# Performance work log

Hardware: AMD Instinct MI355X
Metric: run time of the kernel (lower is better)

Reference implementation:

```python
import jax, jax.numpy as jnp
import numpy as np

# Hard-coded constants from the original module
GAMMA = 0.1      # self.gamma default
N_STEPS = 10     # self.n_steps default
RHO = 0.9        # RMSProp decay
LR = 0.009       # RMSProp learning rate
MOM = 0.9        # momentum
EPS = 1e-8       # RMSProp epsilon
ABS_EPS = 1e-6   # diff_abs smoothing: diff_abs(x) = sqrt(x^2 + 1e-6)

B, IN_DIM, OUT_DIM = 4096, 2048, 4096


def setup_inputs() -> dict:
    key = jax.random.key(0)
    k1, k2 = jax.random.split(key)
    inputs = jax.random.normal(k1, (B, IN_DIM), dtype=jnp.float32)
    # keras 'uniform' init: U(-0.05, 0.05), shape (output_dim, input_dim)
    W = jax.random.uniform(k2, (OUT_DIM, IN_DIM), minval=-0.05, maxval=0.05, dtype=jnp.float32)
    return {"inputs": inputs, "W": W}


def reference(inputs, W):
    batch = inputs.shape[0]
    out_dim = W.shape[0]
    a = jnp.sqrt(inputs * inputs + ABS_EPS)          # diff_abs(inputs), [B, in_dim]
    act = lambda u: 0.5 * (1.0 + jnp.exp(-u))        # self.activation

    def cost(x):
        # l1_norm.sum() + l1_inov + own_norm  (prior = 0)
        l1 = (GAMMA * act(x @ W) * a).sum()
        l1_inov = (GAMMA / 10.0) * jnp.sum(x * x)
        own = GAMMA * jnp.sum(jnp.sqrt(x * x + ABS_EPS))
        return l1 + l1_inov + own

    grad_cost = jax.grad(cost)

    def step(carry, _):
        x, acc1, acc2 = carry
        g = grad_cost(x)                              # [B, out_dim]
        new_acc1 = RHO * acc1 + (1.0 - RHO) * g * g
        denom = jnp.sqrt(new_acc1 + EPS)
        new_acc2 = MOM * acc2 - LR * g / denom
        cand = x - LR * g / denom
        t = 0.1 * LR / denom                          # elementwise prox threshold
        new_x = jnp.maximum(cand - t, 0.0) + jnp.minimum(cand + t, 0.0) + MOM * new_acc2
        new_x = jax.lax.stop_gradient(new_x)          # theano disconnected_grad
        return (new_x, new_acc1, new_acc2), None

    z = jnp.zeros((batch, out_dim), dtype=inputs.dtype)
    # scan runs n_steps; last step's l1_norm uses the state after n_steps-1 updates,
    # so run n_steps-1 updates then compute the final l1_norm directly.
    (x, _, _), _ = jax.lax.scan(step, (z, z, z), None, length=N_STEPS - 1)
    return GAMMA * act(x @ W) * a                     # outputs[-1][-1]: last l1_norm, [B, in_dim]
```

## Files before the change

### kernel.cpp

```cpp
#include <hip/hip_runtime.h>
#include <cstdint>
#include <cstddef>

#define B_DIM   4096
#define IN_DIM  2048
#define OUT_DIM 4096

typedef __attribute__((ext_vector_type(8))) __bf16 bf16x8;
typedef __attribute__((ext_vector_type(4))) float  f32x4;
typedef unsigned short ushortT;

__device__ __forceinline__ ushortT f2bf(float f) {
    unsigned int u = __float_as_uint(f);
    u += 0x7FFFu + ((u >> 16) & 1u);
    return (ushortT)(u >> 16);
}
__device__ __forceinline__ float bf2f(ushortT b) {
    return __uint_as_float(((unsigned int)b) << 16);
}

__device__ __forceinline__ void gload16(const void* g, void* l) {
    __builtin_amdgcn_global_load_lds(
        (const __attribute__((address_space(1))) void*)g,
        (__attribute__((address_space(3))) void*)l, 16, 0, 0);
}

__global__ void prep_g0_kernel(const float* __restrict__ in, ushortT* __restrict__ Gb) {
    int i = blockIdx.x * 256 + threadIdx.x;
    float4 v = reinterpret_cast<const float4*>(in)[i];
    ushort4 g;
    g.x = f2bf(-0.05f * sqrtf(v.x * v.x + 1e-6f));
    g.y = f2bf(-0.05f * sqrtf(v.y * v.y + 1e-6f));
    g.z = f2bf(-0.05f * sqrtf(v.z * v.z + 1e-6f));
    g.w = f2bf(-0.05f * sqrtf(v.w * v.w + 1e-6f));
    reinterpret_cast<ushort4*>(Gb)[i] = g;
}

__global__ void conv_w_kernel(const float* __restrict__ W, ushortT* __restrict__ Wb,
                              ushortT* __restrict__ WTb) {
    __shared__ float tile[64][65];
    const int i0 = blockIdx.x * 64;
    const int j0 = blockIdx.y * 64;
    const int c  = threadIdx.x & 63;
    const int rq = threadIdx.x >> 6;
#pragma unroll
    for (int rp = 0; rp < 16; ++rp) {
        int row = rp * 4 + rq;
        float w = W[(size_t)(j0 + row) * IN_DIM + i0 + c];
        tile[row][c] = w;
        Wb[(size_t)(j0 + row) * IN_DIM + i0 + c] = f2bf(w);
    }
    __syncthreads();
#pragma unroll
    for (int rp = 0; rp < 16; ++rp) {
        int row = rp * 4 + rq;
        WTb[(size_t)(i0 + row) * OUT_DIM + j0 + c] = f2bf(tile[c][row]);
    }
}

template <int EPI, int BM>
__global__ __launch_bounds__(512, 2)
void gemm_ring(const ushortT* __restrict__ A, const ushortT* __restrict__ Bm,
               int N, int K,
               const float* __restrict__ inb, ushortT* __restrict__ Gb,
               float* __restrict__ out,
               float* __restrict__ x, ushortT* __restrict__ acc1,
               ushortT* __restrict__ acc2, ushortT* __restrict__ xb) {
    constexpr int BN   = 256;
    constexpr int ASZ  = BM * 64;
    constexpr int BSZ  = BN * 64;
    constexpr int SLOT = ASZ + BSZ;
    constexpr int LA   = BM / 128;
    constexpr int LB   = BN / 128;
    constexpr int L    = LA + LB;
    constexpr int MR   = BM / 32;
    __shared__ alignas(16) char smem[4 * SLOT];

    const int tid  = threadIdx.x;
    const int lane = tid & 63;
    const int w    = tid >> 6;
    const int wm   = w >> 2;
    const int wn   = w & 3;
    const int nbx  = N / BN;
    const int nwg  = gridDim.x;
    const int cpx  = nwg >> 3;
    const int bid  = (int)blockIdx.x;
    const int swz  = (bid & 7) * cpx + (bid >> 3);
    const int bx   = swz % nbx;
    const int by   = swz / nbx;
    const int row0 = by * BM;
    const int col0 = bx * BN;

    const size_t strideK2 = (size_t)K * 2;

    const char* gAp[LA]; int lAo[LA];
#pragma unroll
    for (int i = 0; i < LA; ++i) {
        int Lp  = i * 512 + tid;
        int row = Lp >> 2, sl = Lp & 3;
        int src = sl ^ ((row >> 1) & 3);
        gAp[i] = (const char*)A + (size_t)(row0 + row) * strideK2 + src * 16;
        lAo[i] = i * 8192 + w * 1024;
    }
    const char* gBp[LB]; int lBo[LB];
#pragma unroll
    for (int i = 0; i < LB; ++i) {
        int Lp  = i * 512 + tid;
        int row = Lp >> 2, sl = Lp & 3;
        int src = sl ^ ((row >> 1) & 3);
        gBp[i] = (const char*)Bm + (size_t)(col0 + row) * strideK2 + src * 16;
        lBo[i] = ASZ + i * 8192 + w * 1024;
    }
    auto stage = [&](int tt) {
        char* sb = smem + (tt & 3) * SLOT;
        const size_t kb = (size_t)tt * 64;
#pragma unroll
        for (int i = 0; i < LA; ++i) gload16(gAp[i] + kb, sb + lAo[i]);
#pragma unroll
        for (int i = 0; i < LB; ++i) gload16(gBp[i] + kb, sb + lBo[i]);
    };

    int aRd[MR], bRd[4];
#pragma unroll
    for (int m = 0; m < MR; ++m) {
        int row = wm * (BM / 2) + m * 16 + (lane & 15);
        aRd[m] = row * 64 + (((lane >> 4) ^ ((row >> 1) & 3)) * 16);
    }
#pragma unroll
    for (int n = 0; n < 4; ++n) {
        int row = wn * 64 + n * 16 + (lane & 15);
        bRd[n] = ASZ + row * 64 + (((lane >> 4) ^ ((row >> 1) & 3)) * 16);
    }

    f32x4 acc[MR][4] = {};

    const int nt = K >> 5;
    stage(0); stage(1); stage(2);

    for (int t = 0; t < nt; ++t) {
        __builtin_amdgcn_s_barrier();
        if (t + 3 < nt) stage(t + 3);
        const int rem = nt - 1 - t;
        if constexpr (L == 4) {
            if (rem >= 3)      asm volatile("s_waitcnt vmcnt(12)" ::: "memory");
            else if (rem == 2) asm volatile("s_waitcnt vmcnt(8)"  ::: "memory");
            else if (rem == 1) asm volatile("s_waitcnt vmcnt(4)"  ::: "memory");
            else               asm volatile("s_waitcnt vmcnt(0)"  ::: "memory");
        } else {
            if (rem >= 3)      asm volatile("s_waitcnt vmcnt(9)"  ::: "memory");
            else if (rem == 2) asm volatile("s_waitcnt vmcnt(6)"  ::: "memory");
            else if (rem == 1) asm volatile("s_waitcnt vmcnt(3)"  ::: "memory");
            else               asm volatile("s_waitcnt vmcnt(0)"  ::: "memory");
        }
        __builtin_amdgcn_s_barrier();

        const char* sb = smem + (t & 3) * SLOT;
        bf16x8 aF[4], bF[4];
#pragma unroll
        for (int n = 0; n < 4; ++n) bF[n] = *reinterpret_cast<const bf16x8*>(sb + bRd[n]);
#pragma unroll
        for (int m = 0; m < 4; ++m) aF[m] = *reinterpret_cast<const bf16x8*>(sb + aRd[m]);
        __builtin_amdgcn_s_setprio(1);
#pragma unroll
        for (int m = 0; m < 4; ++m)
#pragma unroll
            for (int n = 0; n < 4; ++n)
                acc[m][n] = __builtin_amdgcn_mfma_f32_16x16x32_bf16(aF[m], bF[n], acc[m][n], 0, 0, 0);
        __builtin_amdgcn_s_setprio(0);
        if constexpr (MR == 8) {
            bf16x8 aG[4];
#pragma unroll
            for (int m = 0; m < 4; ++m) aG[m] = *reinterpret_cast<const bf16x8*>(sb + aRd[m + 4]);
            __builtin_amdgcn_s_setprio(1);
#pragma unroll
            for (int m = 0; m < 4; ++m)
#pragma unroll
                for (int n = 0; n < 4; ++n)
                    acc[m + 4][n] = __builtin_amdgcn_mfma_f32_16x16x32_bf16(aG[m], bF[n], acc[m + 4][n], 0, 0, 0);
            __builtin_amdgcn_s_setprio(0);
        }
    }

    __builtin_amdgcn_s_barrier();

    float* lep = (float*)(smem + w * 4352);
    const int li = lane >> 4;
    const int lc = lane & 15;
    const int row0w = row0 + wm * (BM / 2);
    const int col0w = col0 + wn * 64;
#pragma unroll
    for (int m = 0; m < MR; ++m) {
#pragma unroll
        for (int n = 0; n < 4; ++n)
#pragma unroll
            for (int i = 0; i < 4; ++i)
                lep[(li * 4 + i) * 68 + n * 16 + lc] = acc[m][n][i];
        asm volatile("s_waitcnt lgkmcnt(0)" ::: "memory");
        __builtin_amdgcn_sched_barrier(0);
#pragma unroll
        for (int rr = 0; rr < 4; ++rr) {
            const int row = rr + li * 4;
            float4 v = *reinterpret_cast<const float4*>(&lep[row * 68 + lc * 4]);
            const size_t idx  = (size_t)(row0w + m * 16 + row) * N + col0w + lc * 4;
            const size_t idx4 = idx >> 2;
            if constexpr (EPI == 0) {
                float4 iv = reinterpret_cast<const float4*>(inb)[idx4];
                ushort4 g;
                g.x = f2bf(-0.05f * sqrtf(iv.x * iv.x + 1e-6f) * expf(-v.x));
                g.y = f2bf(-0.05f * sqrtf(iv.y * iv.y + 1e-6f) * expf(-v.y));
                g.z = f2bf(-0.05f * sqrtf(iv.z * iv.z + 1e-6f) * expf(-v.z));
                g.w = f2bf(-0.05f * sqrtf(iv.w * iv.w + 1e-6f) * expf(-v.w));
                *reinterpret_cast<ushort4*>(&Gb[idx]) = g;
            } else if constexpr (EPI == 1) {
                float4 iv = reinterpret_cast<const float4*>(inb)[idx4];
                float4 o;
                o.x = 0.05f * (1.0f + expf(-v.x)) * sqrtf(iv.x * iv.x + 1e-6f);
                o.y = 0.05f * (1.0f + expf(-v.y)) * sqrtf(iv.y * iv.y + 1e-6f);
                o.z = 0.05f * (1.0f + expf(-v.z)) * sqrtf(iv.z * iv.z + 1e-6f);
                o.w = 0.05f * (1.0f + expf(-v.w)) * sqrtf(iv.w * iv.w + 1e-6f);
                reinterpret_cast<float4*>(out)[idx4] = o;
            } else {
                float4  xv  = reinterpret_cast<const float4*>(x)[idx4];
                ushort4 a1u = *reinterpret_cast<const ushort4*>(&acc1[idx]);
                ushort4 a2u = *reinterpret_cast<const ushort4*>(&acc2[idx]);
                float xs[4] = {xv.x, xv.y, xv.z, xv.w};
                float vs[4] = {v.x, v.y, v.z, v.w};
                ushortT a1s[4] = {a1u.x, a1u.y, a1u.z, a1u.w};
                ushortT a2s[4] = {a2u.x, a2u.y, a2u.z, a2u.w};
                float xn4[4]; ushortT a1n[4], a2n[4], xbn[4];
#pragma unroll
                for (int j = 0; j < 4; ++j) {
                    float g    = vs[j] + 0.02f * xs[j] + 0.1f * xs[j] * rsqrtf(xs[j] * xs[j] + 1e-6f);
                    float a1   = 0.9f * bf2f(a1s[j]) + 0.1f * g * g;
                    float inv  = rsqrtf(a1 + 1e-8f);
                    float r_   = 0.009f * g * inv;
                    float a2   = 0.9f * bf2f(a2s[j]) - r_;
                    float cand = xs[j] - r_;
                    float t_   = 0.0009f * inv;
                    float xn   = fmaxf(cand - t_, 0.0f) + fminf(cand + t_, 0.0f) + 0.9f * a2;
                    xn4[j] = xn; a1n[j] = f2bf(a1); a2n[j] = f2bf(a2); xbn[j] = f2bf(xn);
                }
                float4 xo = {xn4[0], xn4[1], xn4[2], xn4[3]};
                reinterpret_cast<float4*>(x)[idx4] = xo;
                *reinterpret_cast<ushort4*>(&acc1[idx]) = make_ushort4(a1n[0], a1n[1], a1n[2], a1n[3]);
                *reinterpret_cast<ushort4*>(&acc2[idx]) = make_ushort4(a2n[0], a2n[1], a2n[2], a2n[3]);
                *reinterpret_cast<ushort4*>(&xb[idx])   = make_ushort4(xbn[0], xbn[1], xbn[2], xbn[3]);
            }
        }
        asm volatile("s_waitcnt lgkmcnt(0)" ::: "memory");
    }
}

extern "C" void kernel_launch(void* const* d_in, const int* in_sizes, int n_in,
                              void* d_out, int out_size, void* d_ws, size_t ws_size,
                              hipStream_t stream) {
    const float* in = (const float*)d_in[0];
    const float* W  = (const float*)d_in[1];
    float* out = (float*)d_out;
    char* ws = (char*)d_ws;

    float*   x    = (float*)(ws);
    ushortT* acc1 = (ushortT*)(ws + ((size_t)64  << 20));
    ushortT* acc2 = (ushortT*)(ws + ((size_t)96  << 20));
    ushortT* xb   = (ushortT*)(ws + ((size_t)128 << 20));
    ushortT* Wb   = (ushortT*)(ws + ((size_t)160 << 20));
    ushortT* WTb  = (ushortT*)(ws + ((size_t)176 << 20));
    ushortT* Gb   = (ushortT*)(ws + ((size_t)192 << 20));

    hipMemsetAsync(ws, 0, (size_t)128 << 20, stream);

    prep_g0_kernel<<<dim3(B_DIM * IN_DIM / 4 / 256), dim3(256), 0, stream>>>(in, Gb);
    conv_w_kernel<<<dim3(IN_DIM / 64, OUT_DIM / 64), dim3(256), 0, stream>>>(W, Wb, WTb);

    for (int step = 0; step < 9; ++step) {
        if (step > 0) {
            gemm_ring<0, 128><<<dim3(256), dim3(512), 0, stream>>>(
                xb, WTb, IN_DIM, OUT_DIM, in, Gb, nullptr, nullptr, nullptr, nullptr, nullptr);
        }
        gemm_ring<2, 256><<<dim3(256), dim3(512), 0, stream>>>(
            Gb, Wb, OUT_DIM, IN_DIM, nullptr, nullptr, nullptr, x, acc1, acc2, xb);
    }
    gemm_ring<1, 128><<<dim3(256), dim3(512), 0, stream>>>(
        xb, WTb, IN_DIM, OUT_DIM, in, nullptr, out, nullptr, nullptr, nullptr, nullptr);
}
```

Before: 1.716 ms.

## Double-buffer LDS fragments in GEMM loop and drop fp32 x state

Restructures the GEMM main loop so the register fragments for the next k-tile are loaded from LDS while the MFMAs of the current tile run, using two fragment sets and an unroll by two. It also removes the fp32 copy of x and keeps x only in bf16, which cuts epilogue memory traffic and the memset. Launch bounds change from 2 to 1 blocks per CU to leave room for the extra fragment registers. The cost is more register pressure, possibly lower occupancy, and the precision loss of carrying x in bf16 across iterations.

```diff
diff --git a/kernel.cpp b/kernel.cpp
--- a/kernel.cpp
+++ b/kernel.cpp
@@ -59,13 +59,13 @@
 }
 
 template <int EPI, int BM>
-__global__ __launch_bounds__(512, 2)
+__global__ __launch_bounds__(512, 1)
 void gemm_ring(const ushortT* __restrict__ A, const ushortT* __restrict__ Bm,
                int N, int K,
                const float* __restrict__ inb, ushortT* __restrict__ Gb,
                float* __restrict__ out,
-               float* __restrict__ x, ushortT* __restrict__ acc1,
-               ushortT* __restrict__ acc2, ushortT* __restrict__ xb) {
+               ushortT* __restrict__ acc1, ushortT* __restrict__ acc2,
+               ushortT* __restrict__ xb) {
     constexpr int BN   = 256;
     constexpr int ASZ  = BM * 64;
     constexpr int BSZ  = BN * 64;
@@ -133,55 +133,61 @@
     }
 
     f32x4 acc[MR][4] = {};
-
     const int nt = K >> 5;
+
     stage(0); stage(1); stage(2);
-
-    for (int t = 0; t < nt; ++t) {
-        __builtin_amdgcn_s_barrier();
+    asm volatile("s_waitcnt vmcnt(%0)" :: "n"(2 * L) : "memory");
+    __builtin_amdgcn_s_barrier();
+    bf16x8 FA[8], FB[8];
+#pragma unroll
+    for (int m = 0; m < 4; ++m) FA[m]     = *reinterpret_cast<const bf16x8*>(smem + aRd[m]);
+#pragma unroll
+    for (int n = 0; n < 4; ++n) FA[4 + n] = *reinterpret_cast<const bf16x8*>(smem + bRd[n]);
+
+    auto iter = [&](int t, bf16x8 (&cur)[8], bf16x8 (&nxt)[8]) {
         if (t + 3 < nt) stage(t + 3);
         const int rem = nt - 1 - t;
-        if constexpr (L == 4) {
-            if (rem >= 3)      asm volatile("s_waitcnt vmcnt(12)" ::: "memory");
-            else if (rem == 2) asm volatile("s_waitcnt vmcnt(8)"  ::: "memory");
-            else if (rem == 1) asm volatile("s_waitcnt vmcnt(4)"  ::: "memory");
-            else               asm volatile("s_waitcnt vmcnt(0)"  ::: "memory");
-        } else {
-            if (rem >= 3)      asm volatile("s_waitcnt vmcnt(9)"  ::: "memory");
-            else if (rem == 2) asm volatile("s_waitcnt vmcnt(6)"  ::: "memory");
-            else if (rem == 1) asm volatile("s_waitcnt vmcnt(3)"  ::: "memory");
-            else               asm volatile("s_waitcnt vmcnt(0)"  ::: "memory");
-        }
+        if (rem >= 3)      asm volatile("s_waitcnt vmcnt(%0)" :: "n"(2 * L) : "memory");
+        else if (rem == 2) asm volatile("s_waitcnt vmcnt(%0)" :: "n"(L)     : "memory");
+        else               asm volatile("s_waitcnt vmcnt(0)"  ::: "memory");
         __builtin_amdgcn_s_barrier();
-
-        const char* sb = smem + (t & 3) * SLOT;
-        bf16x8 aF[4], bF[4];
-#pragma unroll
-        for (int n = 0; n < 4; ++n) bF[n] = *reinterpret_cast<const bf16x8*>(sb + bRd[n]);
-#pragma unroll
-        for (int m = 0; m < 4; ++m) aF[m] = *reinterpret_cast<const bf16x8*>(sb + aRd[m]);
+        __builtin_amdgcn_sched_barrier(0);
+        const char* sbC = smem + (t & 3) * SLOT;
+        const char* sbN = smem + ((t + 1) & 3) * SLOT;
+        bf16x8 a2[4];
+        if constexpr (MR == 8) {
+#pragma unroll
+            for (int m = 0; m < 4; ++m) a2[m] = *reinterpret_cast<const bf16x8*>(sbC + aRd[m + 4]);
+        }
+        if (rem >= 1) {
+#pragma unroll
+            for (int m = 0; m < 4; ++m) nxt[m]     = *reinterpret_cast<const bf16x8*>(sbN + aRd[m]);
+#pragma unroll
+            for (int n = 0; n < 4; ++n) nxt[4 + n] = *reinterpret_cast<const bf16x8*>(sbN + bRd[n]);
+        }
+        __builtin_amdgcn_sched_barrier(0);
         __builtin_amdgcn_s_setprio(1);
 #pragma unroll
         for (int m = 0; m < 4; ++m)
 #pragma unroll
             for (int n = 0; n < 4; ++n)
-                acc[m][n] = __builtin_amdgcn_mfma_f32_16x16x32_bf16(aF[m], bF[n], acc[m][n], 0, 0, 0);
+                acc[m][n] = __builtin_amdgcn_mfma_f32_16x16x32_bf16(cur[m], cur[4 + n], acc[m][n], 0, 0, 0);
+        if constexpr (MR == 8) {
+#pragma unroll
+            for (int m = 0; m < 4; ++m)
+#pragma unroll
+                for (int n = 0; n < 4; ++n)
+                    acc[m + 4][n] = __builtin_amdgcn_mfma_f32_16x16x32_bf16(a2[m], cur[4 + n], acc[m + 4][n], 0, 0, 0);
+        }
         __builtin_amdgcn_s_setprio(0);
-        if constexpr (MR == 8) {
-            bf16x8 aG[4];
-#pragma unroll
-            for (int m = 0; m < 4; ++m) aG[m] = *reinterpret_cast<const bf16x8*>(sb + aRd[m + 4]);
-            __builtin_amdgcn_s_setprio(1);
-#pragma unroll
-            for (int m = 0; m < 4; ++m)
-#pragma unroll
-                for (int n = 0; n < 4; ++n)
-                    acc[m + 4][n] = __builtin_amdgcn_mfma_f32_16x16x32_bf16(aG[m], bF[n], acc[m + 4][n], 0, 0, 0);
-            __builtin_amdgcn_s_setprio(0);
-        }
-    }
-
-    __builtin_amdgcn_s_barrier();
+        __builtin_amdgcn_s_barrier();
+        __builtin_amdgcn_sched_barrier(0);
+    };
+
+    for (int t = 0; t < nt; t += 2) {
+        iter(t,     FA, FB);
+        iter(t + 1, FB, FA);
+    }
 
     float* lep = (float*)(smem + w * 4352);
     const int li = lane >> 4;
@@ -220,14 +226,14 @@
                 o.w = 0.05f * (1.0f + expf(-v.w)) * sqrtf(iv.w * iv.w + 1e-6f);
                 reinterpret_cast<float4*>(out)[idx4] = o;
             } else {
-                float4  xv  = reinterpret_cast<const float4*>(x)[idx4];
+                ushort4 xu  = *reinterpret_cast<const ushort4*>(&xb[idx]);
                 ushort4 a1u = *reinterpret_cast<const ushort4*>(&acc1[idx]);
                 ushort4 a2u = *reinterpret_cast<const ushort4*>(&acc2[idx]);
-                float xs[4] = {xv.x, xv.y, xv.z, xv.w};
+                float xs[4] = {bf2f(xu.x), bf2f(xu.y), bf2f(xu.z), bf2f(xu.w)};
                 float vs[4] = {v.x, v.y, v.z, v.w};
                 ushortT a1s[4] = {a1u.x, a1u.y, a1u.z, a1u.w};
                 ushortT a2s[4] = {a2u.x, a2u.y, a2u.z, a2u.w};
-                float xn4[4]; ushortT a1n[4], a2n[4], xbn[4];
+                ushortT a1n[4], a2n[4], xbn[4];
 #pragma unroll
                 for (int j = 0; j < 4; ++j) {
                     float g    = vs[j] + 0.02f * xs[j] + 0.1f * xs[j] * rsqrtf(xs[j] * xs[j] + 1e-6f);
@@ -238,10 +244,8 @@
                     float cand = xs[j] - r_;
                     float t_   = 0.0009f * inv;
                     float xn   = fmaxf(cand - t_, 0.0f) + fminf(cand + t_, 0.0f) + 0.9f * a2;
-                    xn4[j] = xn; a1n[j] = f2bf(a1); a2n[j] = f2bf(a2); xbn[j] = f2bf(xn);
+                    a1n[j] = f2bf(a1); a2n[j] = f2bf(a2); xbn[j] = f2bf(xn);
                 }
-                float4 xo = {xn4[0], xn4[1], xn4[2], xn4[3]};
-                reinterpret_cast<float4*>(x)[idx4] = xo;
                 *reinterpret_cast<ushort4*>(&acc1[idx]) = make_ushort4(a1n[0], a1n[1], a1n[2], a1n[3]);
                 *reinterpret_cast<ushort4*>(&acc2[idx]) = make_ushort4(a2n[0], a2n[1], a2n[2], a2n[3]);
                 *reinterpret_cast<ushort4*>(&xb[idx])   = make_ushort4(xbn[0], xbn[1], xbn[2], xbn[3]);
@@ -259,15 +263,14 @@
     float* out = (float*)d_out;
     char* ws = (char*)d_ws;
 
-    float*   x    = (float*)(ws);
-    ushortT* acc1 = (ushortT*)(ws + ((size_t)64  << 20));
-    ushortT* acc2 = (ushortT*)(ws + ((size_t)96  << 20));
-    ushortT* xb   = (ushortT*)(ws + ((size_t)128 << 20));
-    ushortT* Wb   = (ushortT*)(ws + ((size_t)160 << 20));
-    ushortT* WTb  = (ushortT*)(ws + ((size_t)176 << 20));
-    ushortT* Gb   = (ushortT*)(ws + ((size_t)192 << 20));
-
-    hipMemsetAsync(ws, 0, (size_t)128 << 20, stream);
+    ushortT* acc1 = (ushortT*)(ws);
+    ushortT* acc2 = (ushortT*)(ws + ((size_t)32  << 20));
+    ushortT* xb   = (ushortT*)(ws + ((size_t)64  << 20));
+    ushortT* Wb   = (ushortT*)(ws + ((size_t)96  << 20));
+    ushortT* WTb  = (ushortT*)(ws + ((size_t)112 << 20));
+    ushortT* Gb   = (ushortT*)(ws + ((size_t)128 << 20));
+
+    hipMemsetAsync(ws, 0, (size_t)96 << 20, stream);
 
     prep_g0_kernel<<<dim3(B_DIM * IN_DIM / 4 / 256), dim3(256), 0, stream>>>(in, Gb);
     conv_w_kernel<<<dim3(IN_DIM / 64, OUT_DIM / 64), dim3(256), 0, stream>>>(W, Wb, WTb);
@@ -275,11 +278,11 @@
     for (int step = 0; step < 9; ++step) {
         if (step > 0) {
             gemm_ring<0, 128><<<dim3(256), dim3(512), 0, stream>>>(
-                xb, WTb, IN_DIM, OUT_DIM, in, Gb, nullptr, nullptr, nullptr, nullptr, nullptr);
+                xb, WTb, IN_DIM, OUT_DIM, in, Gb, nullptr, nullptr, nullptr, nullptr);
         }
         gemm_ring<2, 256><<<dim3(256), dim3(512), 0, stream>>>(
-            Gb, Wb, OUT_DIM, IN_DIM, nullptr, nullptr, nullptr, x, acc1, acc2, xb);
+            Gb, Wb, OUT_DIM, IN_DIM, nullptr, nullptr, nullptr, acc1, acc2, xb);
     }
     gemm_ring<1, 128><<<dim3(256), dim3(512), 0, stream>>>(
-        xb, WTb, IN_DIM, OUT_DIM, in, nullptr, out, nullptr, nullptr, nullptr, nullptr);
-}
+        xb, WTb, IN_DIM, OUT_DIM, in, nullptr, out, nullptr, nullptr, nullptr);
+}
```

Measured after the change: 1.619 ms. -5.7%, faster.
